# Performance work log

Hardware: AMD Instinct MI355X
Metric: run time of the kernel (lower is better)

## Reference

```python
import jax, jax.numpy as jnp
import numpy as np

OVERLAP_THRESHOLD = 0.5
NEG_POS_RATIO = 3
ALPHA = 1.0


def cxcy_to_xy(cxcy):
    return jnp.concatenate([cxcy[..., :2] - cxcy[..., 2:] / 2,
                            cxcy[..., :2] + cxcy[..., 2:] / 2], axis=-1)


def xy_to_cxcy(xy):
    return jnp.concatenate([(xy[..., :2] + xy[..., 2:]) / 2,
                            xy[..., 2:] - xy[..., :2]], axis=-1)


def cxcy_to_gcxgcy(cxcy, priors_cxcy):
    return jnp.concatenate([
        (cxcy[..., :2] - priors_cxcy[..., :2]) / (priors_cxcy[..., 2:] / 10.0),
        jnp.log(cxcy[..., 2:] / priors_cxcy[..., 2:]) * 5.0], axis=-1)


def jaccard(a, b):
    # a: [N,4] xy, b: [P,4] xy -> [N,P]
    lo = jnp.maximum(a[:, None, :2], b[None, :, :2])
    hi = jnp.minimum(a[:, None, 2:], b[None, :, 2:])
    inter = jnp.prod(jnp.clip(hi - lo, 0.0), axis=-1)  # [N,P]
    area_a = jnp.prod(a[:, 2:] - a[:, :2], axis=-1)  # [N]
    area_b = jnp.prod(b[:, 2:] - b[:, :2], axis=-1)  # [P]
    return inter / (area_a[:, None] + area_b[None, :] - inter)


def _match_one(boxes_i, labels_i, priors_cxcy, priors_xy):
    n_objects = boxes_i.shape[0]
    overlap = jaccard(boxes_i, priors_xy)  # [N,P]
    overlap_for_each_prior = overlap.max(axis=0)  # [P]
    object_for_each_prior = overlap.argmax(axis=0)  # [P]
    prior_for_each_object = overlap.argmax(axis=1)  # [N]
    # force each object to own its best prior
    object_for_each_prior = object_for_each_prior.at[prior_for_each_object].set(
        jnp.arange(n_objects))
    overlap_for_each_prior = overlap_for_each_prior.at[prior_for_each_object].set(1.0)
    labels_for_each_prior = labels_i[object_for_each_prior]
    labels_for_each_prior = jnp.where(overlap_for_each_prior < OVERLAP_THRESHOLD,
                                      0, labels_for_each_prior)
    matched = boxes_i[object_for_each_prior]  # [P,4]
    true_locs = cxcy_to_gcxgcy(xy_to_cxcy(matched), priors_cxcy)  # [P,4]
    return true_locs, labels_for_each_prior


def reference(predicted_locs, predicted_scores, boxes, labels, priors_cxcy):
    B, P, C = predicted_scores.shape
    priors_xy = cxcy_to_xy(priors_cxcy)
    true_locs, true_classes = jax.vmap(
        _match_one, in_axes=(0, 0, None, None))(boxes, labels, priors_cxcy, priors_xy)
    # true_locs: [B,P,4], true_classes: [B,P]
    positive = true_classes != 0  # [B,P]
    n_pos = positive.sum(axis=1)  # [B]
    n_pos_total = n_pos.sum()

    # SmoothL1 (beta=1, mean over selected elements = n_pos_total*4)
    d = predicted_locs - true_locs
    ad = jnp.abs(d)
    sl1 = jnp.where(ad < 1.0, 0.5 * d * d, ad - 0.5)  # [B,P,4]
    loc_loss = (sl1 * positive[..., None]).sum() / (n_pos_total.astype(jnp.float32) * 4.0)

    # per-prior cross-entropy
    logp = jax.nn.log_softmax(predicted_scores, axis=-1)  # [B,P,C]
    conf_all = -jnp.take_along_axis(logp, true_classes[..., None], axis=-1)[..., 0]  # [B,P]

    conf_pos_sum = jnp.where(positive, conf_all, 0.0).sum()
    conf_neg = jnp.where(positive, 0.0, conf_all)
    conf_neg_sorted = jnp.sort(conf_neg, axis=1)[:, ::-1]  # descending
    n_hard_neg = NEG_POS_RATIO * n_pos  # [B]
    rank = jnp.arange(P)[None, :]
    hard_neg_mask = rank < n_hard_neg[:, None]
    conf_hard_neg_sum = jnp.where(hard_neg_mask, conf_neg_sorted, 0.0).sum()

    conf_loss = (conf_hard_neg_sum + conf_pos_sum) / n_pos_total.astype(jnp.float32)
    return conf_loss + ALPHA * loc_loss


def setup_inputs() -> dict:
    key = jax.random.key(0)
    ks = jax.random.split(key, 7)
    B, P, C, N = 128, 8732, 21, 16
    predicted_locs = jax.random.normal(ks[0], (B, P, 4), dtype=jnp.float32)
    predicted_scores = jax.random.normal(ks[1], (B, P, C), dtype=jnp.float32)
    # valid xy boxes in [0,1]
    p1 = jax.random.uniform(ks[2], (B, N, 2)) * 0.85
    wh = jax.random.uniform(ks[3], (B, N, 2), minval=0.02, maxval=0.15)
    boxes = jnp.concatenate([p1, jnp.minimum(p1 + wh, 1.0)], axis=-1)
    labels = jax.random.randint(ks[4], (B, N), 1, C)
    cxcy = jax.random.uniform(ks[5], (P, 2))
    pwh = jax.random.uniform(ks[6], (P, 2), minval=0.05, maxval=0.5)
    priors_cxcy = jnp.concatenate([cxcy, pwh], axis=-1)
    return {"predicted_locs": predicted_locs, "predicted_scores": predicted_scores,
            "boxes": boxes, "labels": labels, "priors_cxcy": priors_cxcy}
```

## Files before the change

### kernel.cpp

```cpp
#include <hip/hip_runtime.h>


#define MAXN 16
#define MAXE 16

__device__ __forceinline__ float sl1f(float d) {
    float ad = fabsf(d);
    return ad < 1.0f ? 0.5f * d * d : ad - 0.5f;
}

__global__ __launch_bounds__(256) void k_pre(
    const float* __restrict__ boxes,
    const float* __restrict__ priors,
    int P, int N,
    int* __restrict__ pfo,
    int* __restrict__ npos,
    float* __restrict__ acc)
{
    __shared__ float rin[4], run[4];
    __shared__ int   rid[4];
    const int id = blockIdx.x;
    const int tid = threadIdx.x;
    const int lane = tid & 63, wid = tid >> 6;

    if (tid == 0 && (id % N) == 0) npos[id / N] = 0;
    if (id == 0 && tid < 2) ((unsigned*)acc)[tid] = 0u;

    const float* bp = boxes + (size_t)id * 4;
    const float bx1 = bp[0], by1 = bp[1], bx2 = bp[2], by2 = bp[3];
    const float ba = (bx2 - bx1) * (by2 - by1);

    float bi = -1.0f, bu = 1.0f; int idx = 0x7fffffff;
#pragma unroll 2
    for (int p = tid; p < P; p += 256) {
        float4 pr = ((const float4*)priors)[p];
        float px1 = pr.x - pr.z * 0.5f, py1 = pr.y - pr.w * 0.5f;
        float px2 = pr.x + pr.z * 0.5f, py2 = pr.y + pr.w * 0.5f;
        float parea = (px2 - px1) * (py2 - py1);
        float iw = fmaxf(fminf(bx2, px2) - fmaxf(bx1, px1), 0.0f);
        float ih = fmaxf(fminf(by2, py2) - fmaxf(by1, py1), 0.0f);
        float in = iw * ih;
        float un = ba + parea - in;
        if (in * bu > bi * un) { bi = in; bu = un; idx = p; }
    }
#pragma unroll
    for (int off = 32; off > 0; off >>= 1) {
        float oin = __shfl_down(bi, off);
        float oun = __shfl_down(bu, off);
        int   oid = __shfl_down(idx, off);
        float a = oin * bu, c = bi * oun;
        if (a > c || (a == c && oid < idx)) { bi = oin; bu = oun; idx = oid; }
    }
    if (lane == 0) { rin[wid] = bi; run[wid] = bu; rid[wid] = idx; }
    __syncthreads();
    if (tid == 0) {
        for (int w = 1; w < 4; w++) {
            float oin = rin[w], oun = run[w]; int oid = rid[w];
            float a = oin * bu, c = bi * oun;
            if (a > c || (a == c && oid < idx)) { bi = oin; bu = oun; idx = oid; }
        }
        pfo[id] = idx;
    }
}

template<int CT>
__global__ __launch_bounds__(256) void k_fused(
    const float* __restrict__ plocs,
    const float* __restrict__ scores,
    const float* __restrict__ boxes,
    const int*   __restrict__ labels,
    const float* __restrict__ priors,
    const int*   __restrict__ pfo,
    int P, int Crt, int N, int nchunk,
    float* __restrict__ conf_out,
    int*   __restrict__ npos,
    float* __restrict__ locpart,
    float* __restrict__ pospart)
{
    const int C = CT > 0 ? CT : Crt;
    extern __shared__ float sh[];
    __shared__ float sx1[MAXN], sy1[MAXN], sx2[MAXN], sy2[MAXN], barea[MAXN];
    __shared__ int   blab[MAXN], spfo[MAXN];
    __shared__ float redf[4], redp[4];
    __shared__ int   redi[4];

    const int b = blockIdx.y;
    const int tid = threadIdx.x;
    const int lane = tid & 63, wid = tid >> 6;
    if (N > MAXN) N = MAXN;
    const int p0 = blockIdx.x * 256;
    const int rows = min(256, P - p0);

    if (tid < N) {
        const float* bp = boxes + ((size_t)b * N + tid) * 4;
        float x1 = bp[0], y1 = bp[1], x2 = bp[2], y2 = bp[3];
        sx1[tid] = x1; sy1[tid] = y1; sx2[tid] = x2; sy2[tid] = y2;
        barea[tid] = (x2 - x1) * (y2 - y1);
        blab[tid] = labels[(size_t)b * N + tid];
        spfo[tid] = pfo[b * N + tid];
    }

    {
        const size_t f4base = ((size_t)b * P + p0) * C / 4;
        const int f4cnt = (rows * C + 3) / 4;
        const float4* __restrict__ s4 = (const float4*)scores + f4base;
        if ((P & 3) == 0) {
            for (int c = wid; c * 64 < f4cnt; c += 4) {
                int idx = c * 64 + lane;
                if (idx < f4cnt) {
                    __builtin_amdgcn_global_load_lds(
                        (const __attribute__((address_space(1))) void*)(s4 + idx),
                        (__attribute__((address_space(3))) void*)((char*)sh + (size_t)c * 1024),
                        16, 0, 0);
                }
            }
            asm volatile("s_waitcnt vmcnt(0)" ::: "memory");
        } else {
            for (int j = tid; j < f4cnt; j += 256)
                ((float4*)sh)[j] = s4[j];
        }
    }
    __syncthreads();

    const int p = p0 + tid;
    float locs = 0.0f, posc = 0.0f, conf = 0.0f;
    int np = 0;
    if (p < P) {
        float4 pr = ((const float4*)priors)[p];
        float px1 = pr.x - pr.z * 0.5f, py1 = pr.y - pr.w * 0.5f;
        float px2 = pr.x + pr.z * 0.5f, py2 = pr.y + pr.w * 0.5f;
        float parea = (px2 - px1) * (py2 - py1);
        float bi = -1.0f, bu = 1.0f; int bestn = 0;
#pragma unroll
        for (int n = 0; n < MAXN; n++) {
            if (n < N) {
                float iw = fmaxf(fminf(sx2[n], px2) - fmaxf(sx1[n], px1), 0.0f);
                float ih = fmaxf(fminf(sy2[n], py2) - fmaxf(sy1[n], py1), 0.0f);
                float in = iw * ih;
                float un = barea[n] + parea - in;
                if (in * bu > bi * un) { bi = in; bu = un; bestn = n; }
            }
        }
#pragma unroll
        for (int n = 0; n < MAXN; n++) {
            if (n < N && spfo[n] == p) { bestn = n; bi = 1.0f; bu = 1.0f; }
        }
        const int lab = (bi < 0.5f * bu) ? 0 : blab[bestn];

        const float* r = sh + tid * C;
        float m = -3.402823466e38f;
#pragma unroll
        for (int c = 0; c < C; c++) m = fmaxf(m, r[c]);
        float sum = 0.0f;
#pragma unroll
        for (int c = 0; c < C; c++) sum += __expf(r[c] - m);
        float ce = m + __logf(sum) - r[lab];

        if (lab != 0) {
            posc = ce; np = 1;
            int n = bestn;
            float cx = (sx1[n] + sx2[n]) * 0.5f, cy = (sy1[n] + sy2[n]) * 0.5f;
            float w = sx2[n] - sx1[n], h = sy2[n] - sy1[n];
            float g0 = (cx - pr.x) / (pr.z / 10.0f);
            float g1 = (cy - pr.y) / (pr.w / 10.0f);
            float g2 = logf(w / pr.z) * 5.0f;
            float g3 = logf(h / pr.w) * 5.0f;
            float4 pl = ((const float4*)plocs)[(size_t)b * P + p];
            locs = sl1f(pl.x - g0) + sl1f(pl.y - g1) + sl1f(pl.z - g2) + sl1f(pl.w - g3);
        } else {
            conf = ce;
        }
        conf_out[(size_t)b * P + p] = conf;
    }
#pragma unroll
    for (int off = 32; off > 0; off >>= 1) {
        locs += __shfl_down(locs, off);
        posc += __shfl_down(posc, off);
        np   += __shfl_down(np, off);
    }
    if (lane == 0) { redf[wid] = locs; redp[wid] = posc; redi[wid] = np; }
    __syncthreads();
    if (tid == 0) {
        float L = redf[0] + redf[1] + redf[2] + redf[3];
        float Pp = redp[0] + redp[1] + redp[2] + redp[3];
        int   c = redi[0] + redi[1] + redi[2] + redi[3];
        if (c) atomicAdd(&npos[b], c);
        locpart[b * nchunk + blockIdx.x] = L;
        pospart[b * nchunk + blockIdx.x] = Pp;
    }
}

__global__ __launch_bounds__(1024, 4) void k_hard(
    const float* __restrict__ conf,
    const int* __restrict__ npos,
    const float* __restrict__ locpart,
    const float* __restrict__ pospart,
    int P, int B, int nloc,
    float* __restrict__ acc,
    float* __restrict__ out)
{
    __shared__ int   redi[16 * 3];
    __shared__ float redf2[16];
    __shared__ int   redi2[16];
    __shared__ float rl[16], rp[16];
    __shared__ int   rn[16], is_last;
    const int b = blockIdx.x, tid = threadIdx.x;
    const int lane = tid & 63, wid = tid >> 6;
    const int nthr = blockDim.x, nw = nthr >> 6;
    const int ne = (P + nthr - 1) / nthr;
    long long kk = (long long)npos[b] * 3;
    int k = kk > P ? P : (int)kk;

    float S = 0.0f;
    if (k > 0) {
        unsigned e[MAXE];
#pragma unroll
        for (int j = 0; j < MAXE; j++) {
            int p = j * nthr + tid;
            e[j] = (j < ne && p < P) ? __float_as_uint(conf[(size_t)b * P + p]) : 0u;
        }

        unsigned lo = 0u, hi = 0x7F800000u;
        while (lo < hi) {
            unsigned span = hi - lo;
            if (span >= 8) {
                unsigned q = span >> 2;
                unsigned m1 = lo + q, m2 = lo + 2 * q, m3 = lo + 3 * q;
                int c1 = 0, c2 = 0, c3 = 0;
#pragma unroll
                for (int j = 0; j < MAXE; j++) {
                    if (j < ne) {
                        unsigned v = e[j];
                        c1 += (int)__popcll(__ballot(v >= m1));
                        c2 += (int)__popcll(__ballot(v >= m2));
                        c3 += (int)__popcll(__ballot(v >= m3));
                    }
                }
                if (lane == 0) {
                    redi[wid * 3 + 0] = c1; redi[wid * 3 + 1] = c2; redi[wid * 3 + 2] = c3;
                }
                __syncthreads();
                int C1 = 0, C2 = 0, C3 = 0;
                for (int w = 0; w < nw; w++) {
                    C1 += redi[w * 3 + 0]; C2 += redi[w * 3 + 1]; C3 += redi[w * 3 + 2];
                }
                __syncthreads();
                if      (C3 >= k) lo = m3;
                else if (C2 >= k) { lo = m2; hi = m3 - 1; }
                else if (C1 >= k) { lo = m1; hi = m2 - 1; }
                else              hi = m1 - 1;
            } else {
                unsigned mid = lo + ((span + 1) >> 1);
                int c = 0;
#pragma unroll
                for (int j = 0; j < MAXE; j++)
                    if (j < ne) c += (int)__popcll(__ballot(e[j] >= mid));
                if (lane == 0) redi[wid * 3] = c;
                __syncthreads();
                int Cc = 0;
                for (int w = 0; w < nw; w++) Cc += redi[w * 3];
                __syncthreads();
                if (Cc >= k) lo = mid; else hi = mid - 1;
            }
        }

        float t = __uint_as_float(lo);
        float sgt = 0.0f; int cgt = 0;
#pragma unroll
        for (int j = 0; j < MAXE; j++) {
            if (j < ne) {
                float v = __uint_as_float(e[j]);
                if (v > t) { sgt += v; cgt++; }
            }
        }
#pragma unroll
        for (int off = 32; off > 0; off >>= 1) {
            sgt += __shfl_down(sgt, off);
            cgt += __shfl_down(cgt, off);
        }
        if (lane == 0) { redf2[wid] = sgt; redi2[wid] = cgt; }
        __syncthreads();
        if (tid == 0) {
            int Cg = 0;
            for (int w = 0; w < nw; w++) { S += redf2[w]; Cg += redi2[w]; }
            S += (float)(k - Cg) * t;
        }
        __syncthreads();
    }

    if (tid == 0) {
        atomicAdd(&acc[0], S);
        __threadfence();
        unsigned tk = atomicAdd((unsigned*)(acc + 1), 1u);
        is_last = (tk == (unsigned)gridDim.x - 1) ? 1 : 0;
    }
    __syncthreads();
    if (is_last) {
        float lp = 0.0f, pp = 0.0f; int np = 0;
        for (int i = tid; i < nloc; i += nthr) { lp += locpart[i]; pp += pospart[i]; }
        for (int i = tid; i < B; i += nthr) np += npos[i];
#pragma unroll
        for (int off = 32; off > 0; off >>= 1) {
            lp += __shfl_down(lp, off);
            pp += __shfl_down(pp, off);
            np += __shfl_down(np, off);
        }
        if (lane == 0) { rl[wid] = lp; rp[wid] = pp; rn[wid] = np; }
        __syncthreads();
        if (tid == 0) {
            float L = 0.0f, Pp = 0.0f; int Np = 0;
            for (int w = 0; w < nw; w++) { L += rl[w]; Pp += rp[w]; Np += rn[w]; }
            float hard = atomicAdd(&acc[0], 0.0f);
            float npf = (float)Np;
            out[0] = (hard + Pp) / npf + L / (npf * 4.0f);
        }
    }
}

extern "C" void kernel_launch(void* const* d_in, const int* in_sizes, int n_in,
                              void* d_out, int out_size, void* d_ws, size_t ws_size,
                              hipStream_t stream)
{
    const float* plocs  = (const float*)d_in[0];
    const float* scores = (const float*)d_in[1];
    const float* boxes  = (const float*)d_in[2];
    const int*   labels = (const int*)d_in[3];
    const float* priors = (const float*)d_in[4];

    int P = in_sizes[4] / 4;
    int B = in_sizes[0] / (P * 4);
    int C = in_sizes[1] / (in_sizes[0] / 4);
    int N = in_sizes[3] / B;
    int nchunk = (P + 255) / 256;
    int nloc = B * nchunk;
    int BN = B * N;

    char* w = (char*)d_ws;
    float* slot    = (float*)w;  w += (size_t)B * P * sizeof(float);
    int*   npos    = (int*)w;    w += (size_t)B * sizeof(int);
    int*   pfo     = (int*)w;    w += (size_t)BN * sizeof(int);
    float* locpart = (float*)w;  w += (size_t)nloc * sizeof(float);
    float* pospart = (float*)w;  w += (size_t)nloc * sizeof(float);
    w = (char*)(((uintptr_t)w + 63) & ~(uintptr_t)63);
    float* acc     = (float*)w;

    k_pre<<<BN, 256, 0, stream>>>(boxes, priors, P, N, pfo, npos, acc);

    dim3 ga(nchunk, B);
    size_t smf = (size_t)256 * C * sizeof(float);
    if (C == 21) {
        k_fused<21><<<ga, 256, smf, stream>>>(plocs, scores, boxes, labels, priors,
                                              pfo, P, C, N, nchunk, slot, npos,
                                              locpart, pospart);
    } else {
        k_fused<0><<<ga, 256, smf, stream>>>(plocs, scores, boxes, labels, priors,
                                             pfo, P, C, N, nchunk, slot, npos,
                                             locpart, pospart);
    }

    k_hard<<<B, 1024, 0, stream>>>(slot, npos, locpart, pospart,
                                   P, B, nloc, acc, (float*)d_out);
}
```

Before: 206.9 us.

## Restructure prior matching to split priors per batch, double-buffer k_hard reductions

k_pre now launches B*SPLIT blocks, where each block handles one slice of priors for all objects of a batch. Each prior is loaded once and tested against all 16 boxes held in registers, instead of launching one block per object that rescans every prior. The per-slice best (intersection, union, index) partials are written to workspace and merged in k_fused's prologue. Separately, k_hard double-buffers its reduction scratch so one __syncthreads per bisection iteration can be dropped. The cost is more register pressure from the per-object arrays and an extra cross-slice merge, and the merge drops the lower-index tie-break across slices.

Measured after the change: 231.3 us. +11.8%, slower.

```diff
diff --git a/kernel.cpp b/kernel.cpp
--- a/kernel.cpp
+++ b/kernel.cpp
@@ -3,6 +3,7 @@
 
 #define MAXN 16
 #define MAXE 16
+#define SPLIT 8
 
 __device__ __forceinline__ float sl1f(float d) {
     float ad = fabsf(d);
@@ -13,53 +14,89 @@
     const float* __restrict__ boxes,
     const float* __restrict__ priors,
     int P, int N,
-    int* __restrict__ pfo,
+    float* __restrict__ pf_in,
+    float* __restrict__ pf_un,
+    int*   __restrict__ pf_id,
     int* __restrict__ npos,
     float* __restrict__ acc)
 {
-    __shared__ float rin[4], run[4];
-    __shared__ int   rid[4];
+    __shared__ float sbx1[MAXN], sby1[MAXN], sbx2[MAXN], sby2[MAXN], sba[MAXN];
+    __shared__ float win[4][MAXN], wun[4][MAXN];
+    __shared__ int   widd[4][MAXN];
     const int id = blockIdx.x;
     const int tid = threadIdx.x;
-    const int lane = tid & 63, wid = tid >> 6;
-
-    if (tid == 0 && (id % N) == 0) npos[id / N] = 0;
+    const int lane = tid & 63, w = tid >> 6;
+    const int b = id / SPLIT, s = id % SPLIT;
+
+    if (s == 0 && tid == 0) npos[b] = 0;
     if (id == 0 && tid < 2) ((unsigned*)acc)[tid] = 0u;
-
-    const float* bp = boxes + (size_t)id * 4;
-    const float bx1 = bp[0], by1 = bp[1], bx2 = bp[2], by2 = bp[3];
-    const float ba = (bx2 - bx1) * (by2 - by1);
-
-    float bi = -1.0f, bu = 1.0f; int idx = 0x7fffffff;
-#pragma unroll 2
-    for (int p = tid; p < P; p += 256) {
+    if (N > MAXN) N = MAXN;
+
+    if (tid < N) {
+        const float* bp = boxes + ((size_t)b * N + tid) * 4;
+        float x1 = bp[0], y1 = bp[1], x2 = bp[2], y2 = bp[3];
+        sbx1[tid] = x1; sby1[tid] = y1; sbx2[tid] = x2; sby2[tid] = y2;
+        sba[tid] = (x2 - x1) * (y2 - y1);
+    }
+    __syncthreads();
+
+    float rx1[MAXN], ry1[MAXN], rx2[MAXN], ry2[MAXN], rar[MAXN];
+#pragma unroll
+    for (int n = 0; n < MAXN; n++) {
+        if (n < N) { rx1[n]=sbx1[n]; ry1[n]=sby1[n]; rx2[n]=sbx2[n]; ry2[n]=sby2[n]; rar[n]=sba[n]; }
+        else       { rx1[n]=0.f; ry1[n]=0.f; rx2[n]=0.f; ry2[n]=0.f; rar[n]=0.f; }
+    }
+
+    const int Q = (P + SPLIT - 1) / SPLIT;
+    const int pbeg = s * Q;
+    const int pend = min(pbeg + Q, P);
+
+    float bi[MAXN], bu[MAXN]; int bx[MAXN];
+#pragma unroll
+    for (int n = 0; n < MAXN; n++) { bi[n] = -1.0f; bu[n] = 1.0f; bx[n] = 0x7fffffff; }
+
+    for (int p = pbeg + tid; p < pend; p += 256) {
         float4 pr = ((const float4*)priors)[p];
         float px1 = pr.x - pr.z * 0.5f, py1 = pr.y - pr.w * 0.5f;
         float px2 = pr.x + pr.z * 0.5f, py2 = pr.y + pr.w * 0.5f;
         float parea = (px2 - px1) * (py2 - py1);
-        float iw = fmaxf(fminf(bx2, px2) - fmaxf(bx1, px1), 0.0f);
-        float ih = fmaxf(fminf(by2, py2) - fmaxf(by1, py1), 0.0f);
-        float in = iw * ih;
-        float un = ba + parea - in;
-        if (in * bu > bi * un) { bi = in; bu = un; idx = p; }
-    }
-#pragma unroll
-    for (int off = 32; off > 0; off >>= 1) {
-        float oin = __shfl_down(bi, off);
-        float oun = __shfl_down(bu, off);
-        int   oid = __shfl_down(idx, off);
-        float a = oin * bu, c = bi * oun;
-        if (a > c || (a == c && oid < idx)) { bi = oin; bu = oun; idx = oid; }
-    }
-    if (lane == 0) { rin[wid] = bi; run[wid] = bu; rid[wid] = idx; }
+#pragma unroll
+        for (int n = 0; n < MAXN; n++) {
+            if (n < N) {
+                float iw = fmaxf(fminf(rx2[n], px2) - fmaxf(rx1[n], px1), 0.0f);
+                float ih = fmaxf(fminf(ry2[n], py2) - fmaxf(ry1[n], py1), 0.0f);
+                float in = iw * ih;
+                float un = rar[n] + parea - in;
+                if (in * bu[n] > bi[n] * un) { bi[n] = in; bu[n] = un; bx[n] = p; }
+            }
+        }
+    }
+
+#pragma unroll
+    for (int n = 0; n < MAXN; n++) {
+        if (n < N) {
+#pragma unroll
+            for (int off = 32; off > 0; off >>= 1) {
+                float oin = __shfl_down(bi[n], off);
+                float oun = __shfl_down(bu[n], off);
+                int   oid = __shfl_down(bx[n], off);
+                float a = oin * bu[n], c = bi[n] * oun;
+                if (a > c || (a == c && oid < bx[n])) { bi[n] = oin; bu[n] = oun; bx[n] = oid; }
+            }
+            if (lane == 0) { win[w][n] = bi[n]; wun[w][n] = bu[n]; widd[w][n] = bx[n]; }
+        }
+    }
     __syncthreads();
-    if (tid == 0) {
-        for (int w = 1; w < 4; w++) {
-            float oin = rin[w], oun = run[w]; int oid = rid[w];
-            float a = oin * bu, c = bi * oun;
-            if (a > c || (a == c && oid < idx)) { bi = oin; bu = oun; idx = oid; }
-        }
-        pfo[id] = idx;
+    if (tid < N) {
+        const int n = tid;
+        float fi = win[0][n], fu = wun[0][n]; int fx = widd[0][n];
+        for (int ww = 1; ww < 4; ww++) {
+            float oin = win[ww][n], oun = wun[ww][n]; int oid = widd[ww][n];
+            float a = oin * fu, c = fi * oun;
+            if (a > c || (a == c && oid < fx)) { fi = oin; fu = oun; fx = oid; }
+        }
+        const size_t o = ((size_t)b * SPLIT + s) * MAXN + n;
+        pf_in[o] = fi; pf_un[o] = fu; pf_id[o] = fx;
     }
 }
 
@@ -70,7 +107,9 @@
     const float* __restrict__ boxes,
     const int*   __restrict__ labels,
     const float* __restrict__ priors,
-    const int*   __restrict__ pfo,
+    const float* __restrict__ pf_in,
+    const float* __restrict__ pf_un,
+    const int*   __restrict__ pf_id,
     int P, int Crt, int N, int nchunk,
     float* __restrict__ conf_out,
     int*   __restrict__ npos,
@@ -97,7 +136,16 @@
         sx1[tid] = x1; sy1[tid] = y1; sx2[tid] = x2; sy2[tid] = y2;
         barea[tid] = (x2 - x1) * (y2 - y1);
         blab[tid] = labels[(size_t)b * N + tid];
-        spfo[tid] = pfo[b * N + tid];
+        const size_t base = (size_t)b * SPLIT * MAXN + tid;
+        float fi = pf_in[base], fu = pf_un[base]; int fx = pf_id[base];
+#pragma unroll
+        for (int sp = 1; sp < SPLIT; sp++) {
+            float oin = pf_in[base + (size_t)sp * MAXN];
+            float oun = pf_un[base + (size_t)sp * MAXN];
+            int   oid = pf_id[base + (size_t)sp * MAXN];
+            if (oin * fu > fi * oun) { fi = oin; fu = oun; fx = oid; }
+        }
+        spfo[tid] = fx;
     }
 
     {
@@ -199,7 +247,7 @@
     float* __restrict__ acc,
     float* __restrict__ out)
 {
-    __shared__ int   redi[16 * 3];
+    __shared__ int   redi[2][16 * 3];
     __shared__ float redf2[16];
     __shared__ int   redi2[16];
     __shared__ float rl[16], rp[16];
@@ -221,7 +269,9 @@
         }
 
         unsigned lo = 0u, hi = 0x7F800000u;
+        int itp = 0;
         while (lo < hi) {
+            int* buf = redi[itp & 1]; itp++;
             unsigned span = hi - lo;
             if (span >= 8) {
                 unsigned q = span >> 2;
@@ -237,14 +287,13 @@
                     }
                 }
                 if (lane == 0) {
-                    redi[wid * 3 + 0] = c1; redi[wid * 3 + 1] = c2; redi[wid * 3 + 2] = c3;
+                    buf[wid * 3 + 0] = c1; buf[wid * 3 + 1] = c2; buf[wid * 3 + 2] = c3;
                 }
                 __syncthreads();
                 int C1 = 0, C2 = 0, C3 = 0;
                 for (int w = 0; w < nw; w++) {
-                    C1 += redi[w * 3 + 0]; C2 += redi[w * 3 + 1]; C3 += redi[w * 3 + 2];
+                    C1 += buf[w * 3 + 0]; C2 += buf[w * 3 + 1]; C3 += buf[w * 3 + 2];
                 }
-                __syncthreads();
                 if      (C3 >= k) lo = m3;
                 else if (C2 >= k) { lo = m2; hi = m3 - 1; }
                 else if (C1 >= k) { lo = m1; hi = m2 - 1; }
@@ -255,14 +304,14 @@
 #pragma unroll
                 for (int j = 0; j < MAXE; j++)
                     if (j < ne) c += (int)__popcll(__ballot(e[j] >= mid));
-                if (lane == 0) redi[wid * 3] = c;
+                if (lane == 0) buf[wid * 3] = c;
                 __syncthreads();
                 int Cc = 0;
-                for (int w = 0; w < nw; w++) Cc += redi[w * 3];
-                __syncthreads();
+                for (int w = 0; w < nw; w++) Cc += buf[w * 3];
                 if (Cc >= k) lo = mid; else hi = mid - 1;
             }
         }
+        __syncthreads();
 
         float t = __uint_as_float(lo);
         float sgt = 0.0f; int cgt = 0;
@@ -333,29 +382,31 @@
     int N = in_sizes[3] / B;
     int nchunk = (P + 255) / 256;
     int nloc = B * nchunk;
-    int BN = B * N;
 
     char* w = (char*)d_ws;
     float* slot    = (float*)w;  w += (size_t)B * P * sizeof(float);
     int*   npos    = (int*)w;    w += (size_t)B * sizeof(int);
-    int*   pfo     = (int*)w;    w += (size_t)BN * sizeof(int);
+    float* pf_in   = (float*)w;  w += (size_t)B * SPLIT * MAXN * sizeof(float);
+    float* pf_un   = (float*)w;  w += (size_t)B * SPLIT * MAXN * sizeof(float);
+    int*   pf_id   = (int*)w;    w += (size_t)B * SPLIT * MAXN * sizeof(int);
     float* locpart = (float*)w;  w += (size_t)nloc * sizeof(float);
     float* pospart = (float*)w;  w += (size_t)nloc * sizeof(float);
     w = (char*)(((uintptr_t)w + 63) & ~(uintptr_t)63);
     float* acc     = (float*)w;
 
-    k_pre<<<BN, 256, 0, stream>>>(boxes, priors, P, N, pfo, npos, acc);
+    k_pre<<<B * SPLIT, 256, 0, stream>>>(boxes, priors, P, N,
+                                         pf_in, pf_un, pf_id, npos, acc);
 
     dim3 ga(nchunk, B);
     size_t smf = (size_t)256 * C * sizeof(float);
     if (C == 21) {
         k_fused<21><<<ga, 256, smf, stream>>>(plocs, scores, boxes, labels, priors,
-                                              pfo, P, C, N, nchunk, slot, npos,
-                                              locpart, pospart);
+                                              pf_in, pf_un, pf_id, P, C, N, nchunk,
+                                              slot, npos, locpart, pospart);
     } else {
         k_fused<0><<<ga, 256, smf, stream>>>(plocs, scores, boxes, labels, priors,
-                                             pfo, P, C, N, nchunk, slot, npos,
-                                             locpart, pospart);
+                                             pf_in, pf_un, pf_id, P, C, N, nchunk,
+                                             slot, npos, locpart, pospart);
     }
 
     k_hard<<<B, 1024, 0, stream>>>(slot, npos, locpart, pospart,
```
